# Kernel optimization log

Hardware: AMD Instinct MI355X
Metric: run time of the kernel (lower is better)

## Reference

```python
import jax, jax.numpy as jnp
import numpy as np

# Geometry (LLaMA-7B-like attention)
B, H, S, D = 1, 32, 2048, 128
NUM_ELEM = B * H * S * D
NUM_OUTLIERS = NUM_ELEM // 256   # outlier_ratio = 1/256 -> 32768 outliers
SINK_LENGTH = 4                  # first 4 tokens of V kept in full precision
QMAX = 7.0                       # symmetric int4: values in [-8, 7]
EPS = 1e-6


def setup_inputs() -> dict:
    key = jax.random.key(0)
    kq, kk, kv = jax.random.split(key, 3)
    q = jax.random.normal(kq, (B, H, S, D), dtype=jnp.float32)
    k = jax.random.normal(kk, (B, H, S, D), dtype=jnp.float32)
    v = jax.random.normal(kv, (B, H, S, D), dtype=jnp.float32)
    return {"q": q, "k": k, "v": v}


def _isolate(x):
    """Split x into dense (outliers zeroed) + sparse (top-|x| values, flat indices)."""
    flat = x.reshape(-1)
    _, idx = jax.lax.top_k(jnp.abs(flat), NUM_OUTLIERS)
    sp_val = flat[idx]
    dense = flat.at[idx].set(0.0).reshape(x.shape)
    return dense, sp_val, idx


def _sink_flat_indices():
    # flat indices of v[:, :, :SINK_LENGTH, :] in row-major [B,H,S,D] layout
    b = jnp.arange(B)[:, None, None, None]
    h = jnp.arange(H)[None, :, None, None]
    s = jnp.arange(SINK_LENGTH)[None, None, :, None]
    d = jnp.arange(D)[None, None, None, :]
    return (((b * H + h) * S + s) * D + d).reshape(-1)


def _quant_dequant(x, scale):
    # symmetric round-to-nearest int4 quantize, then dequantize
    q = jnp.clip(jnp.round(x / scale), -8.0, QMAX)
    return q * scale


def reference(q, k, v):
    # 1) Outlier isolation (K along tokens, V along channels; both flattened scatter)
    k_dense, k_sp_val, k_sp_idx = _isolate(k)
    v_dense, v_sp_val, v_sp_idx = _isolate(v)

    # 2) Sink-token isolation for V (chunk_idx == 0 path): zero sinks in dense,
    #    append their fp values/indices to the sparse set
    sink_idx = _sink_flat_indices()
    v_flat = v.reshape(-1)
    sink_values = v_flat[sink_idx]
    v_dense = v_dense.reshape(-1).at[sink_idx].set(0.0).reshape(v.shape)
    v_sp_val = jnp.concatenate([v_sp_val, sink_values])
    v_sp_idx = jnp.concatenate([v_sp_idx, sink_idx])

    # 3) Per-(head, channel) scale stats (EMA init == first-chunk max |.|)
    k_scale = jnp.maximum(jnp.max(jnp.abs(k_dense), axis=(0, 2), keepdims=True), EPS) / QMAX
    v_scale = jnp.maximum(jnp.max(jnp.abs(v_dense), axis=(0, 2), keepdims=True), EPS) / QMAX

    # 4) Quantize dense part, then reconstruct cache entries: dequant + sparse restore
    k_rec = _quant_dequant(k_dense, k_scale)
    v_rec = _quant_dequant(v_dense, v_scale)
    k_rec = k_rec.reshape(-1).at[k_sp_idx].set(k_sp_val).reshape(k.shape)
    v_rec = v_rec.reshape(-1).at[v_sp_idx].set(v_sp_val).reshape(v.shape)

    # 5) Causal attention over reconstructed KV cache
    scale = 1.0 / np.sqrt(D).astype(np.float32)
    scores = jnp.einsum('bhqd,bhkd->bhqk', q, k_rec) * scale
    causal = jnp.tril(jnp.ones((S, S), dtype=bool))
    scores = jnp.where(causal[None, None], scores, jnp.finfo(scores.dtype).min)
    attn = jax.nn.softmax(scores, axis=-1)
    out = jnp.einsum('bhqk,bhkd->bhqd', attn, v_rec)
    return out
```

## Files before the change

### kernel.cpp

```cpp
#include <hip/hip_runtime.h>

typedef unsigned short u16;
typedef unsigned int u32;
typedef unsigned long long u64;
typedef __attribute__((ext_vector_type(8))) short short8;
typedef __attribute__((ext_vector_type(4))) float f32x4;

#define N_ELEM 8388608
#define NH 32
#define SEQ 2048
#define HD 128
#define KTOP 32768u
#define CAND_CAP 8192u

__device__ __forceinline__ u16 f2bf(float f) {
  union { float f; u32 u; } v; v.f = f;
  u32 r = v.u + 0x7fffu + ((v.u >> 16) & 1u);
  return (u16)(r >> 16);
}

__device__ __forceinline__ float dqf(float x, u32 t, u64 Kr, u32 idx, bool sink, float scale) {
  union { float f; u32 u; } w; w.f = x;
  const u32 ab = w.u & 0x7fffffffu;
  const u32 bin = ab >> 16;
  const bool keep = sink || (bin > t) ||
                    (bin == t && ((((u64)ab) << 32) | (u32)(~idx)) >= Kr);
  if (keep) return x;
  float q = rintf(x / scale);
  q = fminf(fmaxf(q, -8.0f), 7.0f);
  return q * scale;
}

__device__ __forceinline__ u32 cvtpk_bf16(float lo, float hi) {
  u32 r;
  asm("v_cvt_pk_bf16_f32 %0, %1, %2" : "=v"(r) : "v"(lo), "v"(hi));
  return r;
}

__device__ __forceinline__ float bperm_f(int ibyte, float x) {
  union { float f; int i; } a, b;
  a.f = x;
  b.i = __builtin_amdgcn_ds_bpermute(ibyte, a.i);
  return b.f;
}

__global__ __launch_bounds__(256) void hist_kernel(const float* __restrict__ k,
                                                   const float* __restrict__ v,
                                                   u32* __restrict__ histK,
                                                   u32* __restrict__ histV) {
  __shared__ u32 sh[16384];
  const int tensor = blockIdx.x >> 7;
  const int bid = blockIdx.x & 127;
  const float* src = tensor ? v : k;
  u32* gh = tensor ? histV : histK;
  for (int i = threadIdx.x; i < 16384; i += 256) sh[i] = 0;
  __syncthreads();
  const int per = N_ELEM / 128;
  const int base = bid * per;
  for (int i = threadIdx.x; i < per / 4; i += 256) {
    f32x4 x = *(const f32x4*)(src + base + i * 4);
#pragma unroll
    for (int j = 0; j < 4; ++j) {
      union { float f; u32 u; } w; w.f = x[j];
      u32 b = (w.u & 0x7fffffffu) >> 16;
      atomicAdd(&sh[b >> 1], 1u << ((b & 1u) * 16));
    }
  }
  __syncthreads();
  for (int i = threadIdx.x; i < 16384; i += 256) {
    u32 w = sh[i];
    u32 lo = w & 0xffffu, hi = w >> 16;
    if (lo) atomicAdd(&gh[2 * i], lo);
    if (hi) atomicAdd(&gh[2 * i + 1], hi);
  }
}

__global__ __launch_bounds__(256) void thresh_kernel(const u32* __restrict__ histK,
                                                     const u32* __restrict__ histV,
                                                     u32* __restrict__ ctrl) {
  const u32* hist = blockIdx.x ? histV : histK;
  u32* c = ctrl + blockIdx.x * 8;
  __shared__ u32 part[256];
  __shared__ u32 bins[128];
  __shared__ u32 sh_chunk, sh_cum;
  u32 s = 0;
  for (int i = 0; i < 128; ++i) s += hist[threadIdx.x * 128 + i];
  part[threadIdx.x] = s;
  __syncthreads();
  if (threadIdx.x == 0) {
    u32 cum = 0;
    int chunk = 255;
    while (chunk > 0 && cum + part[chunk] < KTOP) { cum += part[chunk]; --chunk; }
    sh_chunk = (u32)chunk; sh_cum = cum;
  }
  __syncthreads();
  const u32 chunk = sh_chunk;
  if (threadIdx.x < 128) bins[threadIdx.x] = hist[chunk * 128 + threadIdx.x];
  __syncthreads();
  if (threadIdx.x == 0) {
    u32 cum = sh_cum;
    int b = 127;
    while (b > 0 && cum + bins[b] < KTOP) { cum += bins[b]; --b; }
    c[0] = chunk * 128 + (u32)b;
    c[1] = KTOP - cum;
  }
}

__global__ __launch_bounds__(256) void candmax_kernel(const float* __restrict__ k,
                                                      const float* __restrict__ v,
                                                      u32* __restrict__ ctrl,
                                                      u32* __restrict__ caK, u32* __restrict__ ciK,
                                                      u32* __restrict__ caV, u32* __restrict__ ciV,
                                                      u32* __restrict__ kmax,
                                                      u32* __restrict__ vmax) {
  __shared__ u32 colmax[128];
  const int tensor = blockIdx.y;
  const float* src = tensor ? v : k;
  u32* ca = tensor ? caV : caK;
  u32* ci = tensor ? ciV : ciK;
  u32* cnt = &ctrl[tensor * 8 + 4];
  u32* mbuf = tensor ? vmax : kmax;
  const u32 t = ctrl[tensor * 8 + 0];
  const int h = blockIdx.x >> 3;
  const int q8 = blockIdx.x & 7;
  const int tid = threadIdx.x;
  if (tid < 128) colmax[tid] = 0;
  __syncthreads();
  const int c0 = 4 * (tid & 31);
  u32 mx[4] = {0, 0, 0, 0};
  for (int p = 0; p < 32; ++p) {
    const int s = q8 * 256 + p * 8 + (tid >> 5);
    const u32 idx = ((u32)(h * SEQ + s) << 7) + (u32)c0;
    f32x4 x = *(const f32x4*)(src + idx);
    const bool skipmax = (tensor == 1 && s < 4);
#pragma unroll
    for (int j = 0; j < 4; ++j) {
      union { float f; u32 u; } w; w.f = x[j];
      const u32 ab = w.u & 0x7fffffffu;
      const u32 bin = ab >> 16;
      if (bin == t) {
        u32 slot = atomicAdd(cnt, 1u);
        if (slot < CAND_CAP) { ca[slot] = ab; ci[slot] = idx + j; }
      }
      if (bin < t && !skipmax && ab > mx[j]) mx[j] = ab;
    }
  }
#pragma unroll
  for (int j = 0; j < 4; ++j) atomicMax(&colmax[c0 + j], mx[j]);
  __syncthreads();
  if (tid < 128) atomicMax(&mbuf[h * HD + tid], colmax[tid]);
}

__global__ __launch_bounds__(256) void ksel_kernel(u32* __restrict__ ctrl,
                                                   const u32* __restrict__ caK, const u32* __restrict__ ciK,
                                                   const u32* __restrict__ caV, const u32* __restrict__ ciV) {
  __shared__ u64 keys[CAND_CAP];
  const int tensor = blockIdx.y;
  u32* c = ctrl + tensor * 8;
  const u32 r = c[1];
  u32 T = c[4];
  if (T > CAND_CAP) T = CAND_CAP;
  const u32* ca = tensor ? caV : caK;
  const u32* ci = tensor ? ciV : ciK;
  for (u32 j = threadIdx.x; j < T; j += 256)
    keys[j] = (((u64)ca[j]) << 32) | (u32)(~ci[j]);
  __syncthreads();
  for (u32 i = blockIdx.x * 256 + threadIdx.x; i < T; i += 32 * 256) {
    const u64 ki = keys[i];
    u32 cnt = 0;
    for (u32 j = 0; j < T; ++j) cnt += (keys[j] > ki) ? 1u : 0u;
    if (cnt == r - 1) { c[2] = (u32)(ki >> 32); c[3] = (u32)ki; }
  }
}

__global__ __launch_bounds__(256) void maxfix_scale_kernel(const u32* __restrict__ ctrl,
                                                           const u32* __restrict__ caK, const u32* __restrict__ ciK,
                                                           const u32* __restrict__ caV, const u32* __restrict__ ciV,
                                                           u32* __restrict__ kmax, u32* __restrict__ vmax,
                                                           float* __restrict__ kscale, float* __restrict__ vscale) {
  const int tensor = blockIdx.x;
  const u32* c = ctrl + tensor * 8;
  const u64 Kr = (((u64)c[2]) << 32) | c[3];
  u32 T = c[4];
  if (T > CAND_CAP) T = CAND_CAP;
  const u32* ca = tensor ? caV : caK;
  const u32* ci = tensor ? ciV : ciK;
  u32* mbuf = tensor ? vmax : kmax;
  for (u32 i = threadIdx.x; i < T; i += 256) {
    const u32 ab = ca[i], idx = ci[i];
    const u64 key = (((u64)ab) << 32) | (u32)(~idx);
    if (key >= Kr) continue;
    if (tensor == 1 && ((idx >> 7) & 2047) < 4) continue;
    atomicMax(&mbuf[(idx >> 18) * HD + (idx & 127)], ab);
  }
  __syncthreads();
  float* sbuf = tensor ? vscale : kscale;
  for (int i = threadIdx.x; i < NH * HD; i += 256) {
    union { u32 u; float f; } a; a.u = mbuf[i];
    sbuf[i] = fmaxf(a.f, 1e-6f) / 7.0f;
  }
}

__global__ __launch_bounds__(256) void recon_kv_kernel(const float* __restrict__ K,
                                                       const float* __restrict__ V,
                                                       const u32* __restrict__ ctrl,
                                                       const float* __restrict__ kscale,
                                                       const float* __restrict__ vscale,
                                                       u16* __restrict__ krec,
                                                       u16* __restrict__ vrecT) {
  __shared__ u32 ld[64][65];
  const int tid = threadIdx.x;
  if (blockIdx.x < 2048) {
    const u32 t = ctrl[0];
    const u64 Kr = (((u64)ctrl[2]) << 32) | ctrl[3];
    const int stride = 2048 * 256;
    for (int i = blockIdx.x * 256 + tid; i < N_ELEM / 4; i += stride) {
      const u32 e = (u32)i * 4;
      const u32 d0 = e & 127, h = e >> 18;
      f32x4 x = *(const f32x4*)(K + e);
      f32x4 sc = *(const f32x4*)(kscale + h * HD + d0);
      u16 y[4];
#pragma unroll
      for (int j = 0; j < 4; ++j) y[j] = f2bf(dqf(x[j], t, Kr, e + j, false, sc[j]));
      *(u32*)(krec + e) = ((u32)y[0]) | (((u32)y[1]) << 16);
      *(u32*)(krec + e + 2) = ((u32)y[2]) | (((u32)y[3]) << 16);
    }
  } else {
    const int b = blockIdx.x - 2048;
    const u32 t = ctrl[8];
    const u64 Kr = (((u64)ctrl[10]) << 32) | ctrl[11];
    const int h = b >> 5, sb = b & 31;
    const int d0 = 4 * (tid & 31);
    f32x4 sc = *(const f32x4*)(vscale + h * HD + d0);
#pragma unroll
    for (int p = 0; p < 8; ++p) {
      const int sl = p * 8 + (tid >> 5);
      const int tok = sb * 64 + sl;
      const bool sink = tok < 4;
      const u32 idx = ((u32)(h * SEQ + tok) << 7) + (u32)d0;
      f32x4 x = *(const f32x4*)(V + idx);
      u16 y[4];
#pragma unroll
      for (int j = 0; j < 4; ++j) y[j] = f2bf(dqf(x[j], t, Kr, idx + j, sink, sc[j]));
      ld[(d0 >> 1)][sl] = ((u32)y[0]) | (((u32)y[1]) << 16);
      ld[(d0 >> 1) + 1][sl] = ((u32)y[2]) | (((u32)y[3]) << 16);
    }
    __syncthreads();
    const int d = tid >> 1, so = (tid & 1) * 32, e = d & 1;
    u16* outp = vrecT + (size_t)(h * 32 + sb) * 8192 + d * 64 + so;
#pragma unroll
    for (int i = 0; i < 4; ++i) {
      short8 y;
#pragma unroll
      for (int m = 0; m < 8; ++m) {
        const u32 w2 = ld[d >> 1][so + i * 8 + m];
        y[m] = (short)(u16)(w2 >> (16 * e));
      }
      *(short8*)(outp + i * 8) = y;
    }
  }
}

#define SC_QK 0.12751743f
#define NEGS -30000.0f

__device__ __forceinline__ void softmax_pack(f32x4 s[4], float& mrow, float& lrow,
                                             u32 pk[8], f32x4& av, bool diag,
                                             int qrow16, int quad, const int* idxR) {
#pragma unroll
  for (int ni = 0; ni < 4; ++ni)
#pragma unroll
    for (int r = 0; r < 4; ++r) {
      float sv = s[ni][r] * SC_QK;
      const int tokl = ((ni >> 1) << 5) | (quad << 3) | ((ni & 1) << 2) | r;
      if (diag && tokl > qrow16) sv = NEGS;
      s[ni][r] = sv;
    }
  float m01 = fmaxf(fmaxf(fmaxf(s[0][0], s[0][1]), fmaxf(s[0][2], s[0][3])),
                    fmaxf(fmaxf(s[1][0], s[1][1]), fmaxf(s[1][2], s[1][3])));
  float m23 = fmaxf(fmaxf(fmaxf(s[2][0], s[2][1]), fmaxf(s[2][2], s[2][3])),
                    fmaxf(fmaxf(s[3][0], s[3][1]), fmaxf(s[3][2], s[3][3])));
  float mx = fmaxf(m01, m23);
  mx = fmaxf(mx, __shfl_xor(mx, 16));
  mx = fmaxf(mx, __shfl_xor(mx, 32));
  const float mn = fmaxf(mrow, mx);
  const float al = exp2f(mrow - mn);
  mrow = mn;
  float sum = 0.f;
#pragma unroll
  for (int ni = 0; ni < 4; ++ni)
#pragma unroll
    for (int r = 0; r < 4; ++r) {
      const float p = exp2f(s[ni][r] - mn);
      s[ni][r] = p;
      sum += p;
    }
  sum += __shfl_xor(sum, 16);
  sum += __shfl_xor(sum, 32);
  lrow = lrow * al + sum;
#pragma unroll
  for (int ni = 0; ni < 4; ++ni) {
    pk[ni * 2] = cvtpk_bf16(s[ni][0], s[ni][1]);
    pk[ni * 2 + 1] = cvtpk_bf16(s[ni][2], s[ni][3]);
  }
#pragma unroll
  for (int r = 0; r < 4; ++r) av[r] = bperm_f(idxR[r], al);
}

__global__ __launch_bounds__(512, 4) void flash_pre(const float* __restrict__ Q,
                                                    const u16* __restrict__ krec,
                                                    const u16* __restrict__ vrecT,
                                                    float* __restrict__ Out) {
  __shared__ u16 ks[64][132];
  __shared__ u16 vt[128][68];

  const int b = blockIdx.x;
  const int h = (b & 7) + 8 * ((b >> 3) >> 4);
  const int pa = (b >> 3) & 15;
  const int RA = pa << 6;
  const int RB = (31 - pa) << 6;
  const int tid = threadIdx.x;
  const int w = tid >> 6, lane = tid & 63;
  const int ww = w & 3;
  const int R = (w >> 2) ? RB : RA;
  const int l16 = lane & 15, quad = lane >> 4;
  const int qrow16 = ww * 16 + l16;

  int idxR[4];
#pragma unroll
  for (int r = 0; r < 4; ++r) idxR[r] = ((lane & 48) | (quad * 4 + r)) << 2;

  short8 qf[4];
  {
    const float* qp = Q + ((size_t)(h * SEQ + R + ww * 16 + l16)) * HD + quad * 8;
#pragma unroll
    for (int c = 0; c < 4; ++c) {
      f32x4 a = *(const f32x4*)(qp + c * 32);
      f32x4 bb = *(const f32x4*)(qp + c * 32 + 4);
      union { u32 u[4]; short8 v; } t;
      t.u[0] = cvtpk_bf16(a[0], a[1]);
      t.u[1] = cvtpk_bf16(a[2], a[3]);
      t.u[2] = cvtpk_bf16(bb[0], bb[1]);
      t.u[3] = cvtpk_bf16(bb[2], bb[3]);
      qf[c] = t.v;
    }
  }

  f32x4 o[8];
#pragma unroll
  for (int i = 0; i < 8; ++i) o[i] = (f32x4){0.f, 0.f, 0.f, 0.f};
  float mrow = NEGS, lrow = 0.f;

  const int krow = tid >> 3, kqo = (tid & 7) * 16;
  const int krp = (krow & 35) | (((krow >> 2) & 1) << 4) |
                  (((krow >> 4) & 1) << 3) | (((krow >> 3) & 1) << 2);
  const int vd = tid >> 2, vco = (tid & 3) * 8;
  const u16* kbase = krec + ((size_t)h * SEQ + krow) * HD + kqo;
  const u16* vbase = vrecT + (size_t)h * 32 * 8192 + vd * 64 + vco;
  short8 kr[2], vr, vr2;
  kr[0] = *(const short8*)(kbase);
  kr[1] = *(const short8*)(kbase + 8);
  vr = *(const short8*)(vbase);
  vr2 = *(const short8*)(vbase + 32);

  const int ktiles = (RB >> 6) + 1;
  for (int kt = 0; kt < ktiles; ++kt) {
    const int kb = kt << 6;
    __syncthreads();
    *(short8*)(&ks[krp][kqo]) = kr[0];
    *(short8*)(&ks[krp][kqo + 8]) = kr[1];
    *(short8*)(&vt[vd][vco]) = vr;
    *(short8*)(&vt[vd][vco + 32]) = vr2;
    __syncthreads();
    if (kt + 1 < ktiles) {
      const u16* kp = kbase + (size_t)(kt + 1) * 64 * HD;
      const u16* vp = vbase + (size_t)(kt + 1) * 8192;
      kr[0] = *(const short8*)(kp);
      kr[1] = *(const short8*)(kp + 8);
      vr = *(const short8*)(vp);
      vr2 = *(const short8*)(vp + 32);
    }
    if (kb <= R) {
      f32x4 s[4];
      __builtin_amdgcn_s_setprio(1);
#pragma unroll
      for (int ni = 0; ni < 4; ++ni) {
        f32x4 acc = (f32x4){0.f, 0.f, 0.f, 0.f};
#pragma unroll
        for (int c = 0; c < 4; ++c) {
          short8 kf = *(const short8*)(&ks[ni * 16 + l16][c * 32 + quad * 8]);
          acc = __builtin_amdgcn_mfma_f32_16x16x32_bf16(kf, qf[c], acc, 0, 0, 0);
        }
        s[ni] = acc;
      }
      __builtin_amdgcn_s_setprio(0);

      u32 pk[8];
      f32x4 av;
      softmax_pack(s, mrow, lrow, pk, av, kb == R, qrow16, quad, idxR);

#pragma unroll
      for (int i = 0; i < 8; ++i) o[i] *= av;

      __builtin_amdgcn_s_setprio(1);
#pragma unroll
      for (int kc = 0; kc < 2; ++kc) {
        union { u32 u[4]; short8 v; } au;
#pragma unroll
        for (int t = 0; t < 4; ++t) au.u[t] = pk[kc * 4 + t];
        const short8 af = au.v;
#pragma unroll
        for (int ds = 0; ds < 8; ++ds) {
          short8 vf = *(const short8*)(&vt[ds * 16 + l16][kc * 32 + quad * 8]);
          o[ds] = __builtin_amdgcn_mfma_f32_16x16x32_bf16(af, vf, o[ds], 0, 0, 0);
        }
      }
      __builtin_amdgcn_s_setprio(0);
    }
  }

  {
    float linv[4];
#pragma unroll
    for (int r = 0; r < 4; ++r) linv[r] = 1.0f / bperm_f(idxR[r], lrow);
#pragma unroll
    for (int r = 0; r < 4; ++r) {
      const int qr = R + ww * 16 + quad * 4 + r;
      float* op = Out + ((size_t)(h * SEQ + qr)) * HD + l16;
#pragma unroll
      for (int ds = 0; ds < 8; ++ds) op[ds * 16] = o[ds][r] * linv[r];
    }
  }
}

__global__ __launch_bounds__(256, 2) void flash_fb(const float* __restrict__ Q,
                                                   const float* __restrict__ K,
                                                   const float* __restrict__ V,
                                                   const u32* __restrict__ ctrl,
                                                   const float* __restrict__ kscale,
                                                   const float* __restrict__ vscale,
                                                   float* __restrict__ Out) {
  __shared__ u16 ks[64][136];
  __shared__ u16 vt[128][72];
  __shared__ u16 pl[4][16][72];
  const int blk = blockIdx.x;
  const int h = blk >> 5;
  const int qt = 31 - (blk & 31);
  const int qb = qt << 6;
  const int tid = threadIdx.x;
  const int w = tid >> 6, lane = tid & 63;
  const int l16 = lane & 15, quad = lane >> 4;
  const float SM_SCALE = 0.08838834764831843f;
  const float NEG = -30000.0f;
  const u32 tK = ctrl[0];
  const u64 KrK = (((u64)ctrl[2]) << 32) | ctrl[3];
  const u32 tV = ctrl[8];
  const u64 KrV = (((u64)ctrl[10]) << 32) | ctrl[11];
  const int cch = (tid & 15) * 8;
  float ksc[8], vsc[8];
#pragma unroll
  for (int j = 0; j < 8; ++j) {
    ksc[j] = kscale[h * HD + cch + j];
    vsc[j] = vscale[h * HD + cch + j];
  }
  short8 qf[4];
  {
    const float* qp = Q + ((size_t)(h * SEQ + qb + w * 16 + l16)) * HD + quad * 8;
#pragma unroll
    for (int c = 0; c < 4; ++c) {
      f32x4 a = *(const f32x4*)(qp + c * 32);
      f32x4 b = *(const f32x4*)(qp + c * 32 + 4);
#pragma unroll
      for (int j = 0; j < 4; ++j) {
        qf[c][j] = (short)f2bf(a[j]);
        qf[c][4 + j] = (short)f2bf(b[j]);
      }
    }
  }
  f32x4 o[8];
#pragma unroll
  for (int i = 0; i < 8; ++i) o[i] = (f32x4){0.f, 0.f, 0.f, 0.f};
  float mrow[4], lrow[4];
#pragma unroll
  for (int r = 0; r < 4; ++r) { mrow[r] = NEG; lrow[r] = 0.f; }
  const int ktiles = qt + 1;
  for (int kt = 0; kt < ktiles; ++kt) {
    const int kb = kt << 6;
    __syncthreads();
    {
      const int r0 = tid >> 4;
      const float* kp = K + (size_t)(h * SEQ + kb) * HD;
#pragma unroll
      for (int i = 0; i < 4; ++i) {
        const int row = r0 + i * 16;
        f32x4 x0 = *(const f32x4*)(kp + (size_t)row * HD + cch);
        f32x4 x1 = *(const f32x4*)(kp + (size_t)row * HD + cch + 4);
        const u32 bidx = ((u32)(h * SEQ + kb + row) << 7) + (u32)cch;
        short8 yv;
#pragma unroll
        for (int j = 0; j < 4; ++j) {
          yv[j]     = (short)f2bf(dqf(x0[j], tK, KrK, bidx + j,     false, ksc[j]));
          yv[4 + j] = (short)f2bf(dqf(x1[j], tK, KrK, bidx + 4 + j, false, ksc[4 + j]));
        }
        *(short8*)(&ks[row][cch]) = yv;
      }
    }
    {
      const float* vp = V + (size_t)(h * SEQ + kb) * HD;
#pragma unroll
      for (int i = 0; i < 4; ++i) {
        const int tchunk = tid + i * 256;
        const int s = tchunk >> 4;
        const int tok = kb + s;
        const bool sink = tok < 4;
        f32x4 x0 = *(const f32x4*)(vp + (size_t)s * HD + cch);
        f32x4 x1 = *(const f32x4*)(vp + (size_t)s * HD + cch + 4);
        const u32 bidx = ((u32)(h * SEQ + tok) << 7) + (u32)cch;
#pragma unroll
        for (int j = 0; j < 4; ++j) {
          vt[cch + j][s]     = f2bf(dqf(x0[j], tV, KrV, bidx + j,     sink, vsc[j]));
          vt[cch + 4 + j][s] = f2bf(dqf(x1[j], tV, KrV, bidx + 4 + j, sink, vsc[4 + j]));
        }
      }
    }
    __syncthreads();
    f32x4 sa[4];
#pragma unroll
    for (int ni = 0; ni < 4; ++ni) {
      f32x4 acc = (f32x4){0.f, 0.f, 0.f, 0.f};
#pragma unroll
      for (int c = 0; c < 4; ++c) {
        short8 kf = *(const short8*)(&ks[ni * 16 + l16][c * 32 + quad * 8]);
        acc = __builtin_amdgcn_mfma_f32_16x16x32_bf16(qf[c], kf, acc, 0, 0, 0);
      }
      sa[ni] = acc;
    }
    const bool diag = (kb == qb);
#pragma unroll
    for (int ni = 0; ni < 4; ++ni)
#pragma unroll
      for (int r = 0; r < 4; ++r) {
        float sv = sa[ni][r] * SM_SCALE;
        if (diag) {
          const int qr = w * 16 + quad * 4 + r;
          const int kc = ni * 16 + l16;
          if (kc > qr) sv = NEG;
        }
        sa[ni][r] = sv;
      }
    float alpha[4];
#pragma unroll
    for (int r = 0; r < 4; ++r) {
      float mx = fmaxf(fmaxf(sa[0][r], sa[1][r]), fmaxf(sa[2][r], sa[3][r]));
      mx = fmaxf(mx, __shfl_xor(mx, 1));
      mx = fmaxf(mx, __shfl_xor(mx, 2));
      mx = fmaxf(mx, __shfl_xor(mx, 4));
      mx = fmaxf(mx, __shfl_xor(mx, 8));
      const float mn = fmaxf(mrow[r], mx);
      alpha[r] = __expf(mrow[r] - mn);
      mrow[r] = mn;
      float sum = 0.f;
#pragma unroll
      for (int ni = 0; ni < 4; ++ni) {
        const float p = __expf(sa[ni][r] - mn);
        sa[ni][r] = p;
        sum += p;
      }
      sum += __shfl_xor(sum, 1);
      sum += __shfl_xor(sum, 2);
      sum += __shfl_xor(sum, 4);
      sum += __shfl_xor(sum, 8);
      lrow[r] = lrow[r] * alpha[r] + sum;
    }
#pragma unroll
    for (int ni = 0; ni < 4; ++ni)
#pragma unroll
      for (int r = 0; r < 4; ++r)
        pl[w][quad * 4 + r][ni * 16 + l16] = f2bf(sa[ni][r]);
    __syncthreads();
#pragma unroll
    for (int i = 0; i < 8; ++i)
#pragma unroll
      for (int r = 0; r < 4; ++r) o[i][r] *= alpha[r];
#pragma unroll
    for (int kc = 0; kc < 2; ++kc) {
      short8 af = *(const short8*)(&pl[w][l16][kc * 32 + quad * 8]);
#pragma unroll
      for (int ds = 0; ds < 8; ++ds) {
        short8 vf = *(const short8*)(&vt[ds * 16 + l16][kc * 32 + quad * 8]);
        o[ds] = __builtin_amdgcn_mfma_f32_16x16x32_bf16(af, vf, o[ds], 0, 0, 0);
      }
    }
  }
#pragma unroll
  for (int r = 0; r < 4; ++r) {
    const float inv = 1.0f / lrow[r];
    const int qr = qb + w * 16 + quad * 4 + r;
    float* op = Out + ((size_t)(h * SEQ + qr)) * HD + l16;
#pragma unroll
    for (int ds = 0; ds < 8; ++ds) op[ds * 16] = o[ds][r] * inv;
  }
}

extern "C" void kernel_launch(void* const* d_in, const int* in_sizes, int n_in,
                              void* d_out, int out_size, void* d_ws, size_t ws_size,
                              hipStream_t stream) {
  const float* q = (const float*)d_in[0];
  const float* k = (const float*)d_in[1];
  const float* v = (const float*)d_in[2];
  float* out = (float*)d_out;
  char* ws = (char*)d_ws;

  u32* ctrl    = (u32*)ws;
  u32* histK   = (u32*)(ws + 256);
  u32* histV   = (u32*)(ws + 256 + 131072);
  u32* kmax    = (u32*)(ws + 262400);
  u32* vmax    = (u32*)(ws + 278784);
  const size_t ZERO_BYTES = 295168;
  float* kscale = (float*)(ws + 295168);
  float* vscale = (float*)(ws + 311552);
  u32* caK = (u32*)(ws + 327936);
  u32* ciK = caK + CAND_CAP;
  u32* caV = ciK + CAND_CAP;
  u32* ciV = caV + CAND_CAP;
  u16* krec  = (u16*)(ws + 458752);
  u16* vrecT = (u16*)(ws + 458752 + 16777216);
  const size_t NEED = 458752 + 2ull * 16777216;

  hipMemsetAsync(ws, 0, ZERO_BYTES, stream);
  hist_kernel<<<256, 256, 0, stream>>>(k, v, histK, histV);
  thresh_kernel<<<2, 256, 0, stream>>>(histK, histV, ctrl);
  candmax_kernel<<<dim3(256, 2), 256, 0, stream>>>(k, v, ctrl, caK, ciK, caV, ciV, kmax, vmax);
  ksel_kernel<<<dim3(32, 2), 256, 0, stream>>>(ctrl, caK, ciK, caV, ciV);
  maxfix_scale_kernel<<<2, 256, 0, stream>>>(ctrl, caK, ciK, caV, ciV, kmax, vmax, kscale, vscale);
  if (ws_size >= NEED) {
    recon_kv_kernel<<<3072, 256, 0, stream>>>(k, v, ctrl, kscale, vscale, krec, vrecT);
    flash_pre<<<512, 512, 0, stream>>>(q, krec, vrecT, out);
  } else {
    flash_fb<<<32 * 32, 256, 0, stream>>>(q, k, v, ctrl, kscale, vscale, out);
  }
}
```

Baseline: 347.2 us.

## Double-buffer K tiles, read V fragments from global, skip lazy softmax rescale

The flash attention kernel now double-buffers K tiles in shared memory, so there is one barrier per tile instead of two. V is no longer staged through LDS; each lane loads its V fragments straight from global memory in the pre-transposed layout. The online softmax also skips the running-max update and the output rescale when every row's new max stays within a threshold of the old one. This cuts LDS traffic and barriers, but V is now read per wave from global/L2 instead of being shared, and the loads may stall the MFMAs.

```diff
diff --git a/kernel.cpp b/kernel.cpp
--- a/kernel.cpp
+++ b/kernel.cpp
@@ -264,55 +264,11 @@
 #define SC_QK 0.12751743f
 #define NEGS -30000.0f
 
-__device__ __forceinline__ void softmax_pack(f32x4 s[4], float& mrow, float& lrow,
-                                             u32 pk[8], f32x4& av, bool diag,
-                                             int qrow16, int quad, const int* idxR) {
-#pragma unroll
-  for (int ni = 0; ni < 4; ++ni)
-#pragma unroll
-    for (int r = 0; r < 4; ++r) {
-      float sv = s[ni][r] * SC_QK;
-      const int tokl = ((ni >> 1) << 5) | (quad << 3) | ((ni & 1) << 2) | r;
-      if (diag && tokl > qrow16) sv = NEGS;
-      s[ni][r] = sv;
-    }
-  float m01 = fmaxf(fmaxf(fmaxf(s[0][0], s[0][1]), fmaxf(s[0][2], s[0][3])),
-                    fmaxf(fmaxf(s[1][0], s[1][1]), fmaxf(s[1][2], s[1][3])));
-  float m23 = fmaxf(fmaxf(fmaxf(s[2][0], s[2][1]), fmaxf(s[2][2], s[2][3])),
-                    fmaxf(fmaxf(s[3][0], s[3][1]), fmaxf(s[3][2], s[3][3])));
-  float mx = fmaxf(m01, m23);
-  mx = fmaxf(mx, __shfl_xor(mx, 16));
-  mx = fmaxf(mx, __shfl_xor(mx, 32));
-  const float mn = fmaxf(mrow, mx);
-  const float al = exp2f(mrow - mn);
-  mrow = mn;
-  float sum = 0.f;
-#pragma unroll
-  for (int ni = 0; ni < 4; ++ni)
-#pragma unroll
-    for (int r = 0; r < 4; ++r) {
-      const float p = exp2f(s[ni][r] - mn);
-      s[ni][r] = p;
-      sum += p;
-    }
-  sum += __shfl_xor(sum, 16);
-  sum += __shfl_xor(sum, 32);
-  lrow = lrow * al + sum;
-#pragma unroll
-  for (int ni = 0; ni < 4; ++ni) {
-    pk[ni * 2] = cvtpk_bf16(s[ni][0], s[ni][1]);
-    pk[ni * 2 + 1] = cvtpk_bf16(s[ni][2], s[ni][3]);
-  }
-#pragma unroll
-  for (int r = 0; r < 4; ++r) av[r] = bperm_f(idxR[r], al);
-}
-
 __global__ __launch_bounds__(512, 4) void flash_pre(const float* __restrict__ Q,
                                                     const u16* __restrict__ krec,
                                                     const u16* __restrict__ vrecT,
                                                     float* __restrict__ Out) {
-  __shared__ u16 ks[64][132];
-  __shared__ u16 vt[128][68];
+  __shared__ u16 ks[2][64][132];
 
   const int b = blockIdx.x;
   const int h = (b & 7) + 8 * ((b >> 3) >> 4);
@@ -354,33 +310,41 @@
   const int krow = tid >> 3, kqo = (tid & 7) * 16;
   const int krp = (krow & 35) | (((krow >> 2) & 1) << 4) |
                   (((krow >> 4) & 1) << 3) | (((krow >> 3) & 1) << 2);
-  const int vd = tid >> 2, vco = (tid & 3) * 8;
   const u16* kbase = krec + ((size_t)h * SEQ + krow) * HD + kqo;
-  const u16* vbase = vrecT + (size_t)h * 32 * 8192 + vd * 64 + vco;
-  short8 kr[2], vr, vr2;
+  const u16* vfb = vrecT + (size_t)h * 32 * 8192 + (size_t)l16 * 64 + quad * 8;
+
+  const int ktiles = (RB >> 6) + 1;
+
+  short8 kr[2];
   kr[0] = *(const short8*)(kbase);
   kr[1] = *(const short8*)(kbase + 8);
-  vr = *(const short8*)(vbase);
-  vr2 = *(const short8*)(vbase + 32);
-
-  const int ktiles = (RB >> 6) + 1;
+  *(short8*)(&ks[0][krp][kqo]) = kr[0];
+  *(short8*)(&ks[0][krp][kqo + 8]) = kr[1];
+  if (1 < ktiles) {
+    const u16* kp = kbase + (size_t)64 * HD;
+    kr[0] = *(const short8*)(kp);
+    kr[1] = *(const short8*)(kp + 8);
+  }
+  __syncthreads();
+
+  int cur = 0;
   for (int kt = 0; kt < ktiles; ++kt) {
     const int kb = kt << 6;
-    __syncthreads();
-    *(short8*)(&ks[krp][kqo]) = kr[0];
-    *(short8*)(&ks[krp][kqo + 8]) = kr[1];
-    *(short8*)(&vt[vd][vco]) = vr;
-    *(short8*)(&vt[vd][vco + 32]) = vr2;
-    __syncthreads();
     if (kt + 1 < ktiles) {
-      const u16* kp = kbase + (size_t)(kt + 1) * 64 * HD;
-      const u16* vp = vbase + (size_t)(kt + 1) * 8192;
+      *(short8*)(&ks[cur ^ 1][krp][kqo]) = kr[0];
+      *(short8*)(&ks[cur ^ 1][krp][kqo + 8]) = kr[1];
+    }
+    if (kt + 2 < ktiles) {
+      const u16* kp = kbase + (size_t)(kt + 2) * 64 * HD;
       kr[0] = *(const short8*)(kp);
       kr[1] = *(const short8*)(kp + 8);
-      vr = *(const short8*)(vp);
-      vr2 = *(const short8*)(vp + 32);
     }
     if (kb <= R) {
+      const u16* vp = vfb + (size_t)kt * 8192;
+      short8 vf[8];
+#pragma unroll
+      for (int ds = 0; ds < 8; ++ds) vf[ds] = *(const short8*)(vp + ds * 1024);
+
       f32x4 s[4];
       __builtin_amdgcn_s_setprio(1);
 #pragma unroll
@@ -388,35 +352,81 @@
         f32x4 acc = (f32x4){0.f, 0.f, 0.f, 0.f};
 #pragma unroll
         for (int c = 0; c < 4; ++c) {
-          short8 kf = *(const short8*)(&ks[ni * 16 + l16][c * 32 + quad * 8]);
+          short8 kf = *(const short8*)(&ks[cur][ni * 16 + l16][c * 32 + quad * 8]);
           acc = __builtin_amdgcn_mfma_f32_16x16x32_bf16(kf, qf[c], acc, 0, 0, 0);
         }
         s[ni] = acc;
       }
       __builtin_amdgcn_s_setprio(0);
 
+      const bool diag = (kb == R);
+#pragma unroll
+      for (int ni = 0; ni < 4; ++ni)
+#pragma unroll
+        for (int r = 0; r < 4; ++r) {
+          float sv = s[ni][r] * SC_QK;
+          const int tokl = ((ni >> 1) << 5) | (quad << 3) | ((ni & 1) << 2) | r;
+          if (diag && tokl > qrow16) sv = NEGS;
+          s[ni][r] = sv;
+        }
+      float m01 = fmaxf(fmaxf(fmaxf(s[0][0], s[0][1]), fmaxf(s[0][2], s[0][3])),
+                        fmaxf(fmaxf(s[1][0], s[1][1]), fmaxf(s[1][2], s[1][3])));
+      float m23 = fmaxf(fmaxf(fmaxf(s[2][0], s[2][1]), fmaxf(s[2][2], s[2][3])),
+                        fmaxf(fmaxf(s[3][0], s[3][1]), fmaxf(s[3][2], s[3][3])));
+      float mx = fmaxf(m01, m23);
+      mx = fmaxf(mx, __shfl_xor(mx, 16));
+      mx = fmaxf(mx, __shfl_xor(mx, 32));
+      const bool skip = (__ballot(mx <= mrow + 8.0f) == ~0ull);
+      float al = 1.0f;
+      if (!skip) {
+        const float mnew = fmaxf(mrow, mx);
+        al = exp2f(mrow - mnew);
+        mrow = mnew;
+      }
+      float sum = 0.f;
+#pragma unroll
+      for (int ni = 0; ni < 4; ++ni)
+#pragma unroll
+        for (int r = 0; r < 4; ++r) {
+          const float p = exp2f(s[ni][r] - mrow);
+          s[ni][r] = p;
+          sum += p;
+        }
+      sum += __shfl_xor(sum, 16);
+      sum += __shfl_xor(sum, 32);
+      lrow = skip ? (lrow + sum) : (lrow * al + sum);
       u32 pk[8];
-      f32x4 av;
-      softmax_pack(s, mrow, lrow, pk, av, kb == R, qrow16, quad, idxR);
-
-#pragma unroll
-      for (int i = 0; i < 8; ++i) o[i] *= av;
-
+#pragma unroll
+      for (int ni = 0; ni < 4; ++ni) {
+        pk[ni * 2] = cvtpk_bf16(s[ni][0], s[ni][1]);
+        pk[ni * 2 + 1] = cvtpk_bf16(s[ni][2], s[ni][3]);
+      }
+      if (!skip) {
+        f32x4 av;
+#pragma unroll
+        for (int r = 0; r < 4; ++r) av[r] = bperm_f(idxR[r], al);
+#pragma unroll
+        for (int i = 0; i < 8; ++i) o[i] *= av;
+      }
+
+      union { u32 u[4]; short8 v; } a0u, a1u;
+#pragma unroll
+      for (int t = 0; t < 4; ++t) { a0u.u[t] = pk[t]; a1u.u[t] = pk[4 + t]; }
       __builtin_amdgcn_s_setprio(1);
 #pragma unroll
-      for (int kc = 0; kc < 2; ++kc) {
-        union { u32 u[4]; short8 v; } au;
-#pragma unroll
-        for (int t = 0; t < 4; ++t) au.u[t] = pk[kc * 4 + t];
-        const short8 af = au.v;
-#pragma unroll
-        for (int ds = 0; ds < 8; ++ds) {
-          short8 vf = *(const short8*)(&vt[ds * 16 + l16][kc * 32 + quad * 8]);
-          o[ds] = __builtin_amdgcn_mfma_f32_16x16x32_bf16(af, vf, o[ds], 0, 0, 0);
-        }
-      }
+      for (int ds = 0; ds < 8; ++ds)
+        o[ds] = __builtin_amdgcn_mfma_f32_16x16x32_bf16(a0u.v, vf[ds], o[ds], 0, 0, 0);
       __builtin_amdgcn_s_setprio(0);
-    }
+#pragma unroll
+      for (int ds = 0; ds < 8; ++ds) vf[ds] = *(const short8*)(vp + ds * 1024 + 32);
+      __builtin_amdgcn_s_setprio(1);
+#pragma unroll
+      for (int ds = 0; ds < 8; ++ds)
+        o[ds] = __builtin_amdgcn_mfma_f32_16x16x32_bf16(a1u.v, vf[ds], o[ds], 0, 0, 0);
+      __builtin_amdgcn_s_setprio(0);
+    }
+    __syncthreads();
+    cur ^= 1;
   }
 
   {
```

Result: slower. 412.0 us (+18.6%).

## Fuse threshold and scale kernels via last-block pattern; add lazy softmax rescale

Applied to the files above, without the earlier changes.

Folds thresh_kernel into hist_kernel and maxfix_scale_kernel into ksel_kernel. Each uses a last-block-done atomic counter so the final block performs the follow-up work, which removes two kernel launches and their gaps. In the flash kernel the softmax helper is inlined and a lazy rescale is added: when no row max grows by more than 8 (log2 units) across the wave, the running max is kept and the O rescale is skipped. This saves exp and multiply work but relies on unnormalised exponentials staying bounded, and it depends on the ctrl counters at offsets 16-19 being zeroed by the memset.

```diff
diff --git a/kernel.cpp b/kernel.cpp
--- a/kernel.cpp
+++ b/kernel.cpp
@@ -44,11 +44,17 @@
   return b.f;
 }
 
+__device__ __forceinline__ u32 aload(const u32* p) {
+  return __hip_atomic_load(p, __ATOMIC_RELAXED, __HIP_MEMORY_SCOPE_AGENT);
+}
+
 __global__ __launch_bounds__(256) void hist_kernel(const float* __restrict__ k,
                                                    const float* __restrict__ v,
                                                    u32* __restrict__ histK,
-                                                   u32* __restrict__ histV) {
+                                                   u32* __restrict__ histV,
+                                                   u32* __restrict__ ctrl) {
   __shared__ u32 sh[16384];
+  __shared__ u32 lastf, sh_chunk, sh_cum;
   const int tensor = blockIdx.x >> 7;
   const int bid = blockIdx.x & 127;
   const float* src = tensor ? v : k;
@@ -73,18 +79,19 @@
     if (lo) atomicAdd(&gh[2 * i], lo);
     if (hi) atomicAdd(&gh[2 * i + 1], hi);
   }
-}
-
-__global__ __launch_bounds__(256) void thresh_kernel(const u32* __restrict__ histK,
-                                                     const u32* __restrict__ histV,
-                                                     u32* __restrict__ ctrl) {
-  const u32* hist = blockIdx.x ? histV : histK;
-  u32* c = ctrl + blockIdx.x * 8;
-  __shared__ u32 part[256];
-  __shared__ u32 bins[128];
-  __shared__ u32 sh_chunk, sh_cum;
+  __threadfence();
+  __syncthreads();
+  if (threadIdx.x == 0)
+    lastf = (atomicAdd(&ctrl[16 + tensor], 1u) == 127u) ? 1u : 0u;
+  __syncthreads();
+  if (!lastf) return;
+  __threadfence();
+  u32* c = ctrl + tensor * 8;
+  u32* part = sh;
+  u32* bins = sh + 256;
   u32 s = 0;
-  for (int i = 0; i < 128; ++i) s += hist[threadIdx.x * 128 + i];
+  for (int i = 0; i < 128; ++i)
+    s += aload(&gh[threadIdx.x * 128 + i]);
   part[threadIdx.x] = s;
   __syncthreads();
   if (threadIdx.x == 0) {
@@ -95,7 +102,7 @@
   }
   __syncthreads();
   const u32 chunk = sh_chunk;
-  if (threadIdx.x < 128) bins[threadIdx.x] = hist[chunk * 128 + threadIdx.x];
+  if (threadIdx.x < 128) bins[threadIdx.x] = aload(&gh[chunk * 128 + threadIdx.x]);
   __syncthreads();
   if (threadIdx.x == 0) {
     u32 cum = sh_cum;
@@ -153,8 +160,11 @@
 
 __global__ __launch_bounds__(256) void ksel_kernel(u32* __restrict__ ctrl,
                                                    const u32* __restrict__ caK, const u32* __restrict__ ciK,
-                                                   const u32* __restrict__ caV, const u32* __restrict__ ciV) {
+                                                   const u32* __restrict__ caV, const u32* __restrict__ ciV,
+                                                   u32* __restrict__ kmax, u32* __restrict__ vmax,
+                                                   float* __restrict__ kscale, float* __restrict__ vscale) {
   __shared__ u64 keys[CAND_CAP];
+  __shared__ u32 lastf;
   const int tensor = blockIdx.y;
   u32* c = ctrl + tensor * 8;
   const u32 r = c[1];
@@ -171,32 +181,27 @@
     for (u32 j = 0; j < T; ++j) cnt += (keys[j] > ki) ? 1u : 0u;
     if (cnt == r - 1) { c[2] = (u32)(ki >> 32); c[3] = (u32)ki; }
   }
-}
-
-__global__ __launch_bounds__(256) void maxfix_scale_kernel(const u32* __restrict__ ctrl,
-                                                           const u32* __restrict__ caK, const u32* __restrict__ ciK,
-                                                           const u32* __restrict__ caV, const u32* __restrict__ ciV,
-                                                           u32* __restrict__ kmax, u32* __restrict__ vmax,
-                                                           float* __restrict__ kscale, float* __restrict__ vscale) {
-  const int tensor = blockIdx.x;
-  const u32* c = ctrl + tensor * 8;
-  const u64 Kr = (((u64)c[2]) << 32) | c[3];
-  u32 T = c[4];
-  if (T > CAND_CAP) T = CAND_CAP;
-  const u32* ca = tensor ? caV : caK;
-  const u32* ci = tensor ? ciV : ciK;
+  __threadfence();
+  __syncthreads();
+  if (threadIdx.x == 0)
+    lastf = (atomicAdd(&ctrl[18 + tensor], 1u) == 31u) ? 1u : 0u;
+  __syncthreads();
+  if (!lastf) return;
+  __threadfence();
+  const u64 Kr = (((u64)aload(&c[2])) << 32) | aload(&c[3]);
   u32* mbuf = tensor ? vmax : kmax;
   for (u32 i = threadIdx.x; i < T; i += 256) {
-    const u32 ab = ca[i], idx = ci[i];
-    const u64 key = (((u64)ab) << 32) | (u32)(~idx);
-    if (key >= Kr) continue;
+    const u64 kk = keys[i];
+    const u32 ab = (u32)(kk >> 32);
+    const u32 idx = ~((u32)kk);
+    if (kk >= Kr) continue;
     if (tensor == 1 && ((idx >> 7) & 2047) < 4) continue;
     atomicMax(&mbuf[(idx >> 18) * HD + (idx & 127)], ab);
   }
   __syncthreads();
   float* sbuf = tensor ? vscale : kscale;
   for (int i = threadIdx.x; i < NH * HD; i += 256) {
-    union { u32 u; float f; } a; a.u = mbuf[i];
+    union { u32 u; float f; } a; a.u = aload(&mbuf[i]);
     sbuf[i] = fmaxf(a.f, 1e-6f) / 7.0f;
   }
 }
@@ -264,49 +269,6 @@
 #define SC_QK 0.12751743f
 #define NEGS -30000.0f
 
-__device__ __forceinline__ void softmax_pack(f32x4 s[4], float& mrow, float& lrow,
-                                             u32 pk[8], f32x4& av, bool diag,
-                                             int qrow16, int quad, const int* idxR) {
-#pragma unroll
-  for (int ni = 0; ni < 4; ++ni)
-#pragma unroll
-    for (int r = 0; r < 4; ++r) {
-      float sv = s[ni][r] * SC_QK;
-      const int tokl = ((ni >> 1) << 5) | (quad << 3) | ((ni & 1) << 2) | r;
-      if (diag && tokl > qrow16) sv = NEGS;
-      s[ni][r] = sv;
-    }
-  float m01 = fmaxf(fmaxf(fmaxf(s[0][0], s[0][1]), fmaxf(s[0][2], s[0][3])),
-                    fmaxf(fmaxf(s[1][0], s[1][1]), fmaxf(s[1][2], s[1][3])));
-  float m23 = fmaxf(fmaxf(fmaxf(s[2][0], s[2][1]), fmaxf(s[2][2], s[2][3])),
-                    fmaxf(fmaxf(s[3][0], s[3][1]), fmaxf(s[3][2], s[3][3])));
-  float mx = fmaxf(m01, m23);
-  mx = fmaxf(mx, __shfl_xor(mx, 16));
-  mx = fmaxf(mx, __shfl_xor(mx, 32));
-  const float mn = fmaxf(mrow, mx);
-  const float al = exp2f(mrow - mn);
-  mrow = mn;
-  float sum = 0.f;
-#pragma unroll
-  for (int ni = 0; ni < 4; ++ni)
-#pragma unroll
-    for (int r = 0; r < 4; ++r) {
-      const float p = exp2f(s[ni][r] - mn);
-      s[ni][r] = p;
-      sum += p;
-    }
-  sum += __shfl_xor(sum, 16);
-  sum += __shfl_xor(sum, 32);
-  lrow = lrow * al + sum;
-#pragma unroll
-  for (int ni = 0; ni < 4; ++ni) {
-    pk[ni * 2] = cvtpk_bf16(s[ni][0], s[ni][1]);
-    pk[ni * 2 + 1] = cvtpk_bf16(s[ni][2], s[ni][3]);
-  }
-#pragma unroll
-  for (int r = 0; r < 4; ++r) av[r] = bperm_f(idxR[r], al);
-}
-
 __global__ __launch_bounds__(512, 4) void flash_pre(const float* __restrict__ Q,
                                                     const u16* __restrict__ krec,
                                                     const u16* __restrict__ vrecT,
@@ -395,12 +357,55 @@
       }
       __builtin_amdgcn_s_setprio(0);
 
+      const bool diag = (kb == R);
+#pragma unroll
+      for (int ni = 0; ni < 4; ++ni)
+#pragma unroll
+        for (int r = 0; r < 4; ++r) {
+          float sv = s[ni][r] * SC_QK;
+          const int tokl = ((ni >> 1) << 5) | (quad << 3) | ((ni & 1) << 2) | r;
+          if (diag && tokl > qrow16) sv = NEGS;
+          s[ni][r] = sv;
+        }
+      float m01 = fmaxf(fmaxf(fmaxf(s[0][0], s[0][1]), fmaxf(s[0][2], s[0][3])),
+                        fmaxf(fmaxf(s[1][0], s[1][1]), fmaxf(s[1][2], s[1][3])));
+      float m23 = fmaxf(fmaxf(fmaxf(s[2][0], s[2][1]), fmaxf(s[2][2], s[2][3])),
+                        fmaxf(fmaxf(s[3][0], s[3][1]), fmaxf(s[3][2], s[3][3])));
+      float mx = fmaxf(m01, m23);
+      mx = fmaxf(mx, __shfl_xor(mx, 16));
+      mx = fmaxf(mx, __shfl_xor(mx, 32));
+      const bool skip = (__ballot(mx <= mrow + 8.0f) == ~0ull);
+      float al = 1.0f;
+      if (!skip) {
+        const float mnew = fmaxf(mrow, mx);
+        al = exp2f(mrow - mnew);
+        mrow = mnew;
+      }
+      float sum = 0.f;
+#pragma unroll
+      for (int ni = 0; ni < 4; ++ni)
+#pragma unroll
+        for (int r = 0; r < 4; ++r) {
+          const float p = exp2f(s[ni][r] - mrow);
+          s[ni][r] = p;
+          sum += p;
+        }
+      sum += __shfl_xor(sum, 16);
+      sum += __shfl_xor(sum, 32);
+      lrow = skip ? (lrow + sum) : (lrow * al + sum);
       u32 pk[8];
-      f32x4 av;
-      softmax_pack(s, mrow, lrow, pk, av, kb == R, qrow16, quad, idxR);
-
-#pragma unroll
-      for (int i = 0; i < 8; ++i) o[i] *= av;
+#pragma unroll
+      for (int ni = 0; ni < 4; ++ni) {
+        pk[ni * 2] = cvtpk_bf16(s[ni][0], s[ni][1]);
+        pk[ni * 2 + 1] = cvtpk_bf16(s[ni][2], s[ni][3]);
+      }
+      if (!skip) {
+        f32x4 av;
+#pragma unroll
+        for (int r = 0; r < 4; ++r) av[r] = bperm_f(idxR[r], al);
+#pragma unroll
+        for (int i = 0; i < 8; ++i) o[i] *= av;
+      }
 
       __builtin_amdgcn_s_setprio(1);
 #pragma unroll
@@ -628,11 +633,9 @@
   const size_t NEED = 458752 + 2ull * 16777216;
 
   hipMemsetAsync(ws, 0, ZERO_BYTES, stream);
-  hist_kernel<<<256, 256, 0, stream>>>(k, v, histK, histV);
-  thresh_kernel<<<2, 256, 0, stream>>>(histK, histV, ctrl);
+  hist_kernel<<<256, 256, 0, stream>>>(k, v, histK, histV, ctrl);
   candmax_kernel<<<dim3(256, 2), 256, 0, stream>>>(k, v, ctrl, caK, ciK, caV, ciV, kmax, vmax);
-  ksel_kernel<<<dim3(32, 2), 256, 0, stream>>>(ctrl, caK, ciK, caV, ciV);
-  maxfix_scale_kernel<<<2, 256, 0, stream>>>(ctrl, caK, ciK, caV, ciV, kmax, vmax, kscale, vscale);
+  ksel_kernel<<<dim3(32, 2), 256, 0, stream>>>(ctrl, caK, ciK, caV, ciV, kmax, vmax, kscale, vscale);
   if (ws_size >= NEED) {
     recon_kv_kernel<<<3072, 256, 0, stream>>>(k, v, ctrl, kscale, vscale, krec, vrecT);
     flash_pre<<<512, 512, 0, stream>>>(q, krec, vrecT, out);
```

Result: slower. 378.6 us (+9.1%).
